# Performance work log

Measured on AMD Instinct MI355X. Metric: run time of the kernel, lower is better.

## Reference

```python
import jax, jax.numpy as jnp
import numpy as np

NOT_EPSILON = 1.0
B, S, D = 1, 512, 256


def swishmax(x, axis):
    xexp = x * jnp.exp(x - jnp.max(x, axis=axis, keepdims=True))
    return xexp / (jnp.sum(jnp.abs(xexp), axis=axis, keepdims=True) + NOT_EPSILON)


def setup_inputs() -> dict:
    key = jax.random.key(0)
    ks = jax.random.split(key, 13)
    scale = 1.0 / np.sqrt(D)
    mk = lambda k: jax.random.uniform(k, (D, D), jnp.float32, -scale, scale)
    mb = lambda k: jax.random.uniform(k, (D,), jnp.float32, -scale, scale)
    return {
        "query_tokens": jax.random.normal(ks[0], (B, S, D), jnp.float32),
        "key_tokens": jax.random.normal(ks[1], (B, S, D), jnp.float32),
        "value_tokens": jax.random.normal(ks[2], (B, S, D), jnp.float32),
        "Wk": mk(ks[3]), "bk": mb(ks[4]),
        "Wq": mk(ks[5]), "bq": mb(ks[6]),
        "Wva": mk(ks[7]), "bva": mb(ks[8]),
        "Wl": mk(ks[9]), "bl": mb(ks[10]),
        "Wvo": mk(ks[11]), "bvo": mb(ks[12]),
    }


def reference(query_tokens, key_tokens, value_tokens,
              Wk, bk, Wq, bq, Wva, bva, Wl, bl, Wvo, bvo):
    # residual linear transforms of tokens
    k = key_tokens + key_tokens @ Wk + bk        # [B,S,D]
    q = query_tokens + query_tokens @ Wq + bq    # [B,S,D]
    # batchify: key -> [B,Sk,1,D], query -> [B,1,Sq,D]; outer-product scores
    attention_raw = k[:, :, None, :] * q[:, None, :, :]          # [B,Sk,Sq,D]
    attention_logits = attention_raw + attention_raw @ Wl + bl   # DxD linear on raw scores
    attention_scale = swishmax(attention_logits, axis=-2)        # normalize over query axis (dim -shape_dims)
    v = value_tokens + value_tokens @ Wva + bva  # [B,S,D]
    values_scaled = v[:, :, None, :] * attention_scale           # [B,Sk,Sq,D]
    value_sum = values_scaled.sum(axis=-3)                       # reduce key axis -> [B,Sq,D]
    value_out = value_sum + value_sum @ Wvo + bvo
    return value_out
```

## Files before the change

### kernel.cpp

```cpp
#include <hip/hip_runtime.h>
#include <math.h>

#define S_LEN 512
#define D_DIM 256
#define SLICE (S_LEN * D_DIM)
#define CSHIFT 8.0f

typedef _Float16 half8  __attribute__((ext_vector_type(8)));
typedef _Float16 half4v __attribute__((ext_vector_type(4)));
typedef float   floatx4 __attribute__((ext_vector_type(4)));

__global__ __launch_bounds__(256) void prep_wl(const float* __restrict__ Wl,
                                               _Float16* __restrict__ WlhT)
{
    const int d = blockIdx.x, e = threadIdx.x;
    float v = Wl[e * D_DIM + d] + (e == d ? 1.0f : 0.0f);
    WlhT[d * D_DIM + e] = (_Float16)v;
}

__global__ __launch_bounds__(256) void linres3(
    const float* __restrict__ xk, const float* __restrict__ Wk,
    const float* __restrict__ bk, _Float16* __restrict__ yk16,
    const float* __restrict__ xq, const float* __restrict__ Wq,
    const float* __restrict__ bq, _Float16* __restrict__ yq16,
    const float* __restrict__ xv, const float* __restrict__ Wv,
    const float* __restrict__ bv, float* __restrict__ yv)
{
    __shared__ float xs[4][D_DIM];
    const int r0 = blockIdx.x * 4;
    const int sel = blockIdx.y;
    const float* x = sel == 0 ? xk : (sel == 1 ? xq : xv);
    const float* W = sel == 0 ? Wk : (sel == 1 ? Wq : Wv);
    const float* b = sel == 0 ? bk : (sel == 1 ? bq : bv);

    const int tid = threadIdx.x;
    #pragma unroll
    for (int t = 0; t < 4; ++t) xs[t][tid] = x[(r0 + t) * D_DIM + tid];
    __syncthreads();
    const float bv_ = b[tid];
    float acc[4];
    #pragma unroll
    for (int i = 0; i < 4; ++i) acc[i] = xs[i][tid] + bv_;
    #pragma unroll 4
    for (int e = 0; e < D_DIM; ++e) {
        const float w = W[e * D_DIM + tid];
        #pragma unroll
        for (int i = 0; i < 4; ++i) acc[i] += xs[i][e] * w;
    }
    if (sel == 2) {
        #pragma unroll
        for (int i = 0; i < 4; ++i) yv[(r0 + i) * D_DIM + tid] = acc[i];
    } else {
        _Float16* y16 = sel == 0 ? yk16 : yq16;
        #pragma unroll
        for (int i = 0; i < 4; ++i) y16[(r0 + i) * D_DIM + tid] = (_Float16)acc[i];
    }
}

__global__ __launch_bounds__(256) void linres_sum(
    const float* __restrict__ po, const float* __restrict__ W,
    const float* __restrict__ b, float* __restrict__ y)
{
    __shared__ float xs[4][D_DIM];
    const int tid = threadIdx.x;
    const int r0  = blockIdx.x * 4;
    #pragma unroll
    for (int t = 0; t < 4; ++t) {
        float s = 0.f;
        #pragma unroll
        for (int c = 0; c < 16; ++c)
            s += po[(size_t)c * SLICE + (r0 + t) * D_DIM + tid];
        xs[t][tid] = s;
    }
    __syncthreads();
    const float bv_ = b[tid];
    float acc[4];
    #pragma unroll
    for (int i = 0; i < 4; ++i) acc[i] = xs[i][tid] + bv_;
    #pragma unroll 4
    for (int e = 0; e < D_DIM; ++e) {
        const float w = W[e * D_DIM + tid];
        #pragma unroll
        for (int i = 0; i < 4; ++i) acc[i] += xs[i][e] * w;
    }
    #pragma unroll
    for (int i = 0; i < 4; ++i) y[(r0 + i) * D_DIM + tid] = acc[i];
}

__device__ __forceinline__ void stage_q(const _Float16* __restrict__ qh,
                                        _Float16* __restrict__ Afrag,
                                        int sq0, int tid)
{
    const int i   = tid & 63;
    const int qtr = tid >> 6;
    const int mt = i >> 4, l16 = i & 15;
    const half8* src = (const half8*)(qh + (size_t)(sq0 + i) * D_DIM + qtr * 64);
    #pragma unroll
    for (int u = 0; u < 8; ++u) {
        const int eb   = qtr * 8 + u;
        const int kk   = eb >> 2, quad = eb & 3;
        const int addr16 = (mt * 8 + kk) * 64 + quad * 16 + l16;
        *(half8*)(Afrag + addr16 * 8) = src[u];
    }
}

__device__ __forceinline__ void stage_q32(const _Float16* __restrict__ qh,
                                          _Float16* __restrict__ Afrag,
                                          int sq0, int tid)
{
    const int i   = tid & 31;
    const int oct = tid >> 5;
    const int mt = i >> 4, l16 = i & 15;
    const half8* src = (const half8*)(qh + (size_t)(sq0 + i) * D_DIM);
    #pragma unroll
    for (int u = 0; u < 4; ++u) {
        const int eb   = oct * 4 + u;
        const int kk   = eb >> 2, quad = eb & 3;
        const int addr16 = (mt * 8 + kk) * 64 + quad * 16 + l16;
        *(half8*)(Afrag + addr16 * 8) = src[eb];
    }
}

__global__ __launch_bounds__(256, 2) void stats_mfma(
    const _Float16* __restrict__ qh, const _Float16* __restrict__ kh,
    const _Float16* __restrict__ WlhT, const float* __restrict__ bl,
    float* __restrict__ pm, float* __restrict__ ps)
{
    __shared__ _Float16 Afrag[32 * 64 * 8];

    const int tid  = threadIdx.x;
    const int lane = tid & 63, wave = tid >> 6;
    const int quad = lane >> 4, l16 = lane & 15;
    const int sqt  = blockIdx.x, sq0 = sqt * 64;
    const int dw   = blockIdx.y * 128 + wave * 32;
    const int sk0  = blockIdx.z * 16;

    stage_q(qh, Afrag, sq0, tid);

    half8 wl[2][8];
    #pragma unroll
    for (int nt = 0; nt < 2; ++nt) {
        const int d = dw + nt * 16 + l16;
        #pragma unroll
        for (int kk = 0; kk < 8; ++kk)
            wl[nt][kk] = *(const half8*)(WlhT + (size_t)d * D_DIM + kk * 32 + quad * 8);
    }
    float bl_r[2];
    #pragma unroll
    for (int nt = 0; nt < 2; ++nt)
        bl_r[nt] = bl[dw + nt * 16 + l16];

    __syncthreads();

    #pragma unroll 1
    for (int s2 = 0; s2 < 8; ++s2) {
        const int sk = sk0 + s2 * 2;

        floatx4 acc[2][4][2];
        #pragma unroll
        for (int c = 0; c < 2; ++c)
            #pragma unroll
            for (int mt = 0; mt < 4; ++mt)
                #pragma unroll
                for (int nt = 0; nt < 2; ++nt)
                    acc[c][mt][nt] = (floatx4){0.f, 0.f, 0.f, 0.f};

        #pragma unroll
        for (int kk = 0; kk < 8; ++kk) {
            half8 k8[2];
            #pragma unroll
            for (int c = 0; c < 2; ++c)
                k8[c] = *(const half8*)(kh + (size_t)(sk + c) * D_DIM + kk * 32 + quad * 8);
            half8 af[4];
            #pragma unroll
            for (int mt = 0; mt < 4; ++mt)
                af[mt] = *(const half8*)(Afrag + ((mt * 8 + kk) * 64 + lane) * 8);
            #pragma unroll
            for (int c = 0; c < 2; ++c)
                #pragma unroll
                for (int nt = 0; nt < 2; ++nt) {
                    const half8 bf = wl[nt][kk] * k8[c];
                    #pragma unroll
                    for (int mt = 0; mt < 4; ++mt)
                        acc[c][mt][nt] = __builtin_amdgcn_mfma_f32_16x16x32_f16(
                            af[mt], bf, acc[c][mt][nt], 0, 0, 0);
                }
        }

        #pragma unroll
        for (int c = 0; c < 2; ++c)
            #pragma unroll
            for (int nt = 0; nt < 2; ++nt) {
                float tmax = -1e30f, tsum = 0.f;
                #pragma unroll
                for (int mt = 0; mt < 4; ++mt)
                    #pragma unroll
                    for (int r = 0; r < 4; ++r) {
                        const float L = acc[c][mt][nt][r] + bl_r[nt];
                        tmax = fmaxf(tmax, L);
                        tsum += fabsf(L) * __expf(L - CSHIFT);
                    }
                float m = tmax, ss = tsum;
                #pragma unroll
                for (int mask = 16; mask <= 32; mask <<= 1) {
                    m  = fmaxf(m, __shfl_xor(m, mask, 64));
                    ss += __shfl_xor(ss, mask, 64);
                }
                if (quad == 0) {
                    const int d = dw + nt * 16 + l16;
                    pm[((size_t)sqt * S_LEN + sk + c) * D_DIM + d] = m;
                    ps[((size_t)sqt * S_LEN + sk + c) * D_DIM + d] = ss;
                }
            }
    }
}

__global__ __launch_bounds__(256) void reduce_ms(
    const float* __restrict__ pm, const float* __restrict__ ps,
    const float* __restrict__ vbuf, float* __restrict__ wbuf)
{
    const int idx = blockIdx.x * 256 + threadIdx.x;
    float mv[8], sv[8];
    #pragma unroll
    for (int t = 0; t < 8; ++t) {
        mv[t] = pm[(size_t)t * SLICE + idx];
        sv[t] = ps[(size_t)t * SLICE + idx];
    }
    float M = mv[0];
    #pragma unroll
    for (int t = 1; t < 8; ++t) M = fmaxf(M, mv[t]);
    float S = 0.f;
    #pragma unroll
    for (int t = 0; t < 8; ++t) S += sv[t];
    const float denom = S + __expf(M - CSHIFT);
    wbuf[idx] = vbuf[idx] / denom;
}

__global__ __launch_bounds__(256, 2) void accum_mfma(
    const _Float16* __restrict__ qh, const _Float16* __restrict__ kh,
    const _Float16* __restrict__ WlhT, const float* __restrict__ bl,
    const float* __restrict__ wbuf, float* __restrict__ po)
{
    __shared__ _Float16 Afrag[16 * 64 * 8];

    const int tid  = threadIdx.x;
    const int lane = tid & 63, wave = tid >> 6;
    const int quad = lane >> 4, l16 = lane & 15;
    const int sq0  = blockIdx.x * 32;
    const int dw   = blockIdx.y * 128 + wave * 32;
    const int chunk = blockIdx.z;
    const int sk0  = chunk * 32;

    stage_q32(qh, Afrag, sq0, tid);

    half8 wl[2][8];
    #pragma unroll
    for (int nt = 0; nt < 2; ++nt) {
        const int d = dw + nt * 16 + l16;
        #pragma unroll
        for (int kk = 0; kk < 8; ++kk)
            wl[nt][kk] = *(const half8*)(WlhT + (size_t)d * D_DIM + kk * 32 + quad * 8);
    }
    float bl_r[2];
    #pragma unroll
    for (int nt = 0; nt < 2; ++nt)
        bl_r[nt] = bl[dw + nt * 16 + l16];

    __syncthreads();

    half8 afr[2][8];
    #pragma unroll
    for (int mt = 0; mt < 2; ++mt)
        #pragma unroll
        for (int kk = 0; kk < 8; ++kk)
            afr[mt][kk] = *(const half8*)(Afrag + ((mt * 8 + kk) * 64 + lane) * 8);

    floatx4 o[2][2];
    #pragma unroll
    for (int mt = 0; mt < 2; ++mt)
        #pragma unroll
        for (int nt = 0; nt < 2; ++nt)
            o[mt][nt] = (floatx4){0.f, 0.f, 0.f, 0.f};

    #pragma unroll 1
    for (int s = 0; s < 32; ++s) {
        const int sk = sk0 + s;

        float w_r2[2];
        #pragma unroll
        for (int nt = 0; nt < 2; ++nt)
            w_r2[nt] = wbuf[(size_t)sk * D_DIM + dw + nt * 16 + l16];

        floatx4 acc[2][2];
        #pragma unroll
        for (int mt = 0; mt < 2; ++mt)
            #pragma unroll
            for (int nt = 0; nt < 2; ++nt)
                acc[mt][nt] = (floatx4){0.f, 0.f, 0.f, 0.f};

        #pragma unroll
        for (int kk = 0; kk < 8; ++kk) {
            const half8 k8 = *(const half8*)(kh + (size_t)sk * D_DIM + kk * 32 + quad * 8);
            half8 bf[2];
            #pragma unroll
            for (int nt = 0; nt < 2; ++nt)
                bf[nt] = wl[nt][kk] * k8;
            #pragma unroll
            for (int mt = 0; mt < 2; ++mt)
                #pragma unroll
                for (int nt = 0; nt < 2; ++nt)
                    acc[mt][nt] = __builtin_amdgcn_mfma_f32_16x16x32_f16(
                        afr[mt][kk], bf[nt], acc[mt][nt], 0, 0, 0);
        }

        #pragma unroll
        for (int nt = 0; nt < 2; ++nt) {
            const float w_r = w_r2[nt];
            #pragma unroll
            for (int mt = 0; mt < 2; ++mt)
                #pragma unroll
                for (int r = 0; r < 4; ++r) {
                    const float L = acc[mt][nt][r] + bl_r[nt];
                    o[mt][nt][r] += w_r * (L * __expf(L - CSHIFT));
                }
        }
    }

    float* dst = po + (size_t)chunk * SLICE;
    #pragma unroll
    for (int mt = 0; mt < 2; ++mt)
        #pragma unroll
        for (int nt = 0; nt < 2; ++nt)
            #pragma unroll
            for (int r = 0; r < 4; ++r) {
                const int row = sq0 + mt * 16 + quad * 4 + r;
                const int col = dw + nt * 16 + l16;
                dst[(size_t)row * D_DIM + col] = o[mt][nt][r];
            }
}

extern "C" void kernel_launch(void* const* d_in, const int* in_sizes, int n_in,
                              void* d_out, int out_size, void* d_ws, size_t ws_size,
                              hipStream_t stream)
{
    const float* query = (const float*)d_in[0];
    const float* key   = (const float*)d_in[1];
    const float* value = (const float*)d_in[2];
    const float* Wk  = (const float*)d_in[3];
    const float* bk  = (const float*)d_in[4];
    const float* Wq  = (const float*)d_in[5];
    const float* bq  = (const float*)d_in[6];
    const float* Wva = (const float*)d_in[7];
    const float* bva = (const float*)d_in[8];
    const float* Wl  = (const float*)d_in[9];
    const float* bl  = (const float*)d_in[10];
    const float* Wvo = (const float*)d_in[11];
    const float* bvo = (const float*)d_in[12];

    const int MAT = SLICE;
    float* ws   = (float*)d_ws;
    float* vbuf = ws + 2 * MAT;
    float* wbuf = ws + 3 * MAT;
    _Float16* WlhT = (_Float16*)(ws + 6 * MAT);
    _Float16* kh   = (_Float16*)(ws + 6 * MAT + 32768);
    _Float16* qh   = kh + MAT;
    float* pm  = ws + 6 * MAT + 32768 + 2 * 65536;
    float* ps  = pm + 8 * MAT;
    float* po  = pm;
    float* out = (float*)d_out;

    prep_wl<<<256, 256, 0, stream>>>(Wl, WlhT);
    linres3<<<dim3(128, 3), 256, 0, stream>>>(key, Wk, bk, kh,
                                              query, Wq, bq, qh,
                                              value, Wva, bva, vbuf);

    stats_mfma<<<dim3(8, 2, 32), 256, 0, stream>>>(qh, kh, WlhT, bl, pm, ps);
    reduce_ms<<<512, 256, 0, stream>>>(pm, ps, vbuf, wbuf);
    accum_mfma<<<dim3(16, 2, 16), 256, 0, stream>>>(qh, kh, WlhT, bl,
                                                    wbuf, po);

    linres_sum<<<128, 256, 0, stream>>>(po, Wvo, bvo, out);
}
```

Measured before the change: 240.7 us.

## Fold log2(e) into Wl and bias to use native exp2, restructure stats loop

Pre-scales the fused Wl+I weights and the bias by log2(e) so logits come out in base-2 units. The exponentials can then use the hardware exp2 instruction directly, with no multiply inside __expf. The reduce kernel corrects by ln2 so the normalization stays equivalent. The stats kernel also now handles one key row per iteration instead of two, which lowers accumulator register pressure, and it uses tree-shaped max/sum reductions. The catch is that scaling by log2e before the fp16 cast slightly changes rounding of the weights.

```diff
diff --git a/kernel.cpp b/kernel.cpp
--- a/kernel.cpp
+++ b/kernel.cpp
@@ -4,7 +4,12 @@
 #define S_LEN 512
 #define D_DIM 256
 #define SLICE (S_LEN * D_DIM)
-#define CSHIFT 8.0f
+
+#define LOG2E  1.44269504088896f
+#define LN2    0.69314718055995f
+#define C2     (8.0f * LOG2E)
+
+#define EXP2F(x) __builtin_amdgcn_exp2f(x)
 
 typedef _Float16 half8  __attribute__((ext_vector_type(8)));
 typedef _Float16 half4v __attribute__((ext_vector_type(4)));
@@ -14,7 +19,7 @@
                                                _Float16* __restrict__ WlhT)
 {
     const int d = blockIdx.x, e = threadIdx.x;
-    float v = Wl[e * D_DIM + d] + (e == d ? 1.0f : 0.0f);
+    float v = (Wl[e * D_DIM + d] + (e == d ? 1.0f : 0.0f)) * LOG2E;
     WlhT[d * D_DIM + e] = (_Float16)v;
 }
 
@@ -148,70 +153,68 @@
     float bl_r[2];
     #pragma unroll
     for (int nt = 0; nt < 2; ++nt)
-        bl_r[nt] = bl[dw + nt * 16 + l16];
+        bl_r[nt] = bl[dw + nt * 16 + l16] * LOG2E;
 
     __syncthreads();
 
     #pragma unroll 1
-    for (int s2 = 0; s2 < 8; ++s2) {
-        const int sk = sk0 + s2 * 2;
-
-        floatx4 acc[2][4][2];
-        #pragma unroll
-        for (int c = 0; c < 2; ++c)
+    for (int s = 0; s < 16; ++s) {
+        const int sk = sk0 + s;
+        floatx4 acc[4][2];
+        #pragma unroll
+        for (int mt = 0; mt < 4; ++mt)
+            #pragma unroll
+            for (int nt = 0; nt < 2; ++nt)
+                acc[mt][nt] = (floatx4){0.f, 0.f, 0.f, 0.f};
+
+        #pragma unroll
+        for (int kk = 0; kk < 8; ++kk) {
+            const half8 k8 = *(const half8*)(kh + (size_t)sk * D_DIM + kk * 32 + quad * 8);
+            half8 af[4], bf[2];
+            #pragma unroll
+            for (int mt = 0; mt < 4; ++mt)
+                af[mt] = *(const half8*)(Afrag + ((mt * 8 + kk) * 64 + lane) * 8);
+            #pragma unroll
+            for (int nt = 0; nt < 2; ++nt)
+                bf[nt] = wl[nt][kk] * k8;
             #pragma unroll
             for (int mt = 0; mt < 4; ++mt)
                 #pragma unroll
                 for (int nt = 0; nt < 2; ++nt)
-                    acc[c][mt][nt] = (floatx4){0.f, 0.f, 0.f, 0.f};
-
-        #pragma unroll
-        for (int kk = 0; kk < 8; ++kk) {
-            half8 k8[2];
-            #pragma unroll
-            for (int c = 0; c < 2; ++c)
-                k8[c] = *(const half8*)(kh + (size_t)(sk + c) * D_DIM + kk * 32 + quad * 8);
-            half8 af[4];
-            #pragma unroll
-            for (int mt = 0; mt < 4; ++mt)
-                af[mt] = *(const half8*)(Afrag + ((mt * 8 + kk) * 64 + lane) * 8);
-            #pragma unroll
-            for (int c = 0; c < 2; ++c)
-                #pragma unroll
-                for (int nt = 0; nt < 2; ++nt) {
-                    const half8 bf = wl[nt][kk] * k8[c];
-                    #pragma unroll
-                    for (int mt = 0; mt < 4; ++mt)
-                        acc[c][mt][nt] = __builtin_amdgcn_mfma_f32_16x16x32_f16(
-                            af[mt], bf, acc[c][mt][nt], 0, 0, 0);
-                }
+                    acc[mt][nt] = __builtin_amdgcn_mfma_f32_16x16x32_f16(
+                        af[mt], bf[nt], acc[mt][nt], 0, 0, 0);
         }
 
         #pragma unroll
-        for (int c = 0; c < 2; ++c)
-            #pragma unroll
-            for (int nt = 0; nt < 2; ++nt) {
-                float tmax = -1e30f, tsum = 0.f;
-                #pragma unroll
-                for (int mt = 0; mt < 4; ++mt)
-                    #pragma unroll
-                    for (int r = 0; r < 4; ++r) {
-                        const float L = acc[c][mt][nt][r] + bl_r[nt];
-                        tmax = fmaxf(tmax, L);
-                        tsum += fabsf(L) * __expf(L - CSHIFT);
-                    }
-                float m = tmax, ss = tsum;
-                #pragma unroll
-                for (int mask = 16; mask <= 32; mask <<= 1) {
-                    m  = fmaxf(m, __shfl_xor(m, mask, 64));
-                    ss += __shfl_xor(ss, mask, 64);
-                }
-                if (quad == 0) {
-                    const int d = dw + nt * 16 + l16;
-                    pm[((size_t)sqt * S_LEN + sk + c) * D_DIM + d] = m;
-                    ps[((size_t)sqt * S_LEN + sk + c) * D_DIM + d] = ss;
-                }
+        for (int nt = 0; nt < 2; ++nt) {
+            float mmx[4], tss[4];
+            #pragma unroll
+            for (int mt = 0; mt < 4; ++mt) {
+                float L0 = acc[mt][nt][0] + bl_r[nt];
+                float L1 = acc[mt][nt][1] + bl_r[nt];
+                float L2 = acc[mt][nt][2] + bl_r[nt];
+                float L3 = acc[mt][nt][3] + bl_r[nt];
+                float t0 = fabsf(L0) * EXP2F(L0 - C2);
+                float t1 = fabsf(L1) * EXP2F(L1 - C2);
+                float t2 = fabsf(L2) * EXP2F(L2 - C2);
+                float t3 = fabsf(L3) * EXP2F(L3 - C2);
+                mmx[mt] = fmaxf(fmaxf(L0, L1), fmaxf(L2, L3));
+                tss[mt] = (t0 + t1) + (t2 + t3);
             }
+            float m  = fmaxf(fmaxf(mmx[0], mmx[1]), fmaxf(mmx[2], mmx[3]));
+            float ss = (tss[0] + tss[1]) + (tss[2] + tss[3]);
+
+            #pragma unroll
+            for (int mask = 16; mask <= 32; mask <<= 1) {
+                m  = fmaxf(m, __shfl_xor(m, mask, 64));
+                ss += __shfl_xor(ss, mask, 64);
+            }
+            if (quad == 0) {
+                const int d = dw + nt * 16 + l16;
+                pm[((size_t)sqt * S_LEN + sk) * D_DIM + d] = m;
+                ps[((size_t)sqt * S_LEN + sk) * D_DIM + d] = ss;
+            }
+        }
     }
 }
 
@@ -226,14 +229,12 @@
         mv[t] = pm[(size_t)t * SLICE + idx];
         sv[t] = ps[(size_t)t * SLICE + idx];
     }
-    float M = mv[0];
-    #pragma unroll
-    for (int t = 1; t < 8; ++t) M = fmaxf(M, mv[t]);
-    float S = 0.f;
-    #pragma unroll
-    for (int t = 0; t < 8; ++t) S += sv[t];
-    const float denom = S + __expf(M - CSHIFT);
-    wbuf[idx] = vbuf[idx] / denom;
+    float M = fmaxf(fmaxf(fmaxf(mv[0], mv[1]), fmaxf(mv[2], mv[3])),
+                    fmaxf(fmaxf(mv[4], mv[5]), fmaxf(mv[6], mv[7])));
+    float S = ((sv[0] + sv[1]) + (sv[2] + sv[3]))
+            + ((sv[4] + sv[5]) + (sv[6] + sv[7]));
+    const float denom = S * LN2 + EXP2F(M - C2);
+    wbuf[idx] = vbuf[idx] * (LN2 / denom);
 }
 
 __global__ __launch_bounds__(256, 2) void accum_mfma(
@@ -264,7 +265,7 @@
     float bl_r[2];
     #pragma unroll
     for (int nt = 0; nt < 2; ++nt)
-        bl_r[nt] = bl[dw + nt * 16 + l16];
+        bl_r[nt] = bl[dw + nt * 16 + l16] * LOG2E;
 
     __syncthreads();
 
@@ -320,8 +321,8 @@
             for (int mt = 0; mt < 2; ++mt)
                 #pragma unroll
                 for (int r = 0; r < 4; ++r) {
-                    const float L = acc[mt][nt][r] + bl_r[nt];
-                    o[mt][nt][r] += w_r * (L * __expf(L - CSHIFT));
+                    const float L2 = acc[mt][nt][r] + bl_r[nt];
+                    o[mt][nt][r] += w_r * (L2 * EXP2F(L2 - C2));
                 }
         }
     }
```

New measurement: 216.5 us. -10.1%, faster.
